# Kernel optimization log

Measured on AMD Instinct MI355X. Metric: run time of the kernel, lower is better.

The kernel has to match this reference:

```python
import jax, jax.numpy as jnp
import numpy as np

B, S, D = 4, 2048, 1024
H, HK = 16, 4          # num_heads, num_heads_kv
HD = D // H            # head_dim = 64
G = H // HK            # kv groups = 4


def setup_inputs() -> dict:
    key = jax.random.key(0)
    ks = jax.random.split(key, 7)
    s = 0.02
    return {
        "query": jax.random.normal(ks[0], (B, S, D), jnp.float32),
        "key":   jax.random.normal(ks[1], (B, S, D), jnp.float32),
        "value": jax.random.normal(ks[2], (B, S, D), jnp.float32),
        # weights stored (in, out); equivalent to torch Linear y = x @ W.T
        "Wq": jax.random.normal(ks[3], (D, H * HD), jnp.float32) * s,
        "Wk": jax.random.normal(ks[4], (D, HK * HD), jnp.float32) * s,
        "Wv": jax.random.normal(ks[5], (D, HK * HD), jnp.float32) * s,
        "Wo": jax.random.normal(ks[6], (H * HD, D), jnp.float32) * s,
    }


def reference(query, key, value, Wq, Wk, Wv, Wo):
    b, qlen, _ = query.shape
    kvlen = key.shape[1]
    # projections
    q = (query @ Wq).reshape(b, qlen, H, HD)        # [b,q,H,hd]
    k = (key @ Wk).reshape(b, kvlen, HK, HD)        # [b,s,HK,hd]
    v = (value @ Wv).reshape(b, kvlen, HK, HD)      # [b,s,HK,hd]
    # GQA: q head h attends kv head h//G (repeat_interleave semantics)
    qg = q.reshape(b, qlen, HK, G, HD)              # head = kv*G + group
    scale = 1.0 / jnp.sqrt(jnp.asarray(HD, q.dtype))
    # scores [b,HK,G,q,s] -- broadcast kv heads, no materialized repeat
    scores = jnp.einsum('bqkgd,bskd->bkgqs', qg, k) * scale
    attn = jax.nn.softmax(scores, axis=-1)
    out = jnp.einsum('bkgqs,bskd->bqkgd', attn, v)  # [b,q,HK,G,hd]
    out = out.reshape(b, qlen, H * HD)
    return out @ Wo
```

## Files before the change

kernel.cpp:

```cpp
#include <hip/hip_runtime.h>


typedef unsigned short u16;
typedef unsigned int   u32;
typedef __bf16 bf16x4 __attribute__((ext_vector_type(4)));
typedef __bf16 bf16x8 __attribute__((ext_vector_type(8)));
typedef float  f32x4  __attribute__((ext_vector_type(4)));

#define MFMA(a,b,c) __builtin_amdgcn_mfma_f32_16x16x32_bf16((a),(b),(c),0,0,0)

#define GLDS(g, l) __builtin_amdgcn_global_load_lds(                          \
    (const __attribute__((address_space(1))) void*)(g),                       \
    (__attribute__((address_space(3))) void*)(l), 16, 0, 0)

#if __has_builtin(__builtin_amdgcn_exp2f)
#define EXP2(x) __builtin_amdgcn_exp2f(x)
#else
#define EXP2(x) exp2f(x)
#endif

__device__ __forceinline__ u16 f2bf(float f){
    u32 u = __builtin_bit_cast(u32, f);
    u += 0x7fffu + ((u >> 16) & 1u);
    return (u16)(u >> 16);
}
__device__ __forceinline__ u32 pk2(float a, float b){
#if __has_builtin(__builtin_amdgcn_cvt_pk_bf16_f32)
    auto r = __builtin_amdgcn_cvt_pk_bf16_f32(a, b);
    return __builtin_bit_cast(u32, r);
#else
    return (u32)f2bf(a) | ((u32)f2bf(b) << 16);
#endif
}
__device__ __forceinline__ bf16x8 ldfrag(const u16* p){
    return *(const bf16x8*)p;
}
__device__ __forceinline__ bf16x8 ld2x64(const u16* p){
    bf16x4 lo = *(const bf16x4*)p;
    bf16x4 hi = *(const bf16x4*)(p + 4);
    bf16x8 r;
    r[0]=lo[0]; r[1]=lo[1]; r[2]=lo[2]; r[3]=lo[3];
    r[4]=hi[0]; r[5]=hi[1]; r[6]=hi[2]; r[7]=hi[3];
    return r;
}

__global__ __launch_bounds__(256) void prep(const float* __restrict__ Wq,
                                            const float* __restrict__ Wk,
                                            const float* __restrict__ Wv,
                                            const float* __restrict__ Wo,
                                            u16* WqT, u16* WkT, u16* WvT, u16* WoT){
    const int tid = threadIdx.x, bid = blockIdx.x;
    __shared__ float T[32][33];
    const float* W; u16* WT; int N, i;
    if (bid < 1024)      { W = Wq; WT = WqT; N = 1024; i = bid; }
    else if (bid < 1280) { W = Wk; WT = WkT; N =  256; i = bid - 1024; }
    else if (bid < 1536) { W = Wv; WT = WvT; N =  256; i = bid - 1280; }
    else                 { W = Wo; WT = WoT; N = 1024; i = bid - 1536; }
    int kt = (i & 31) * 32, nt = (i >> 5) * 32;
    int r = tid >> 3, c = tid & 7;
    float4 vv = *(const float4*)(W + (size_t)(kt + r) * N + nt + c * 4);
    T[r][c*4+0] = vv.x; T[r][c*4+1] = vv.y; T[r][c*4+2] = vv.z; T[r][c*4+3] = vv.w;
    __syncthreads();
    u32 lo = pk2(T[c*4+0][r], T[c*4+1][r]);
    u32 hi = pk2(T[c*4+2][r], T[c*4+3][r]);
    *(uint2*)(WT + (size_t)(nt + r) * 1024 + kt + c * 4) = make_uint2(lo, hi);
}

template<int ATYPE, int EPI>
__device__ __forceinline__ void gemm_body(const void* __restrict__ Ap,
                                          const u16* __restrict__ Bt,
                                          void* __restrict__ Cp,
                                          int N, int K, int m0, int n0,
                                          u16* As, u16* Bs, float oscale){
    constexpr int ASTR = (ATYPE == 0) ? 80 : 64;
    const int tid  = threadIdx.x;
    const int wave = tid >> 6, lane = tid & 63;
    const int quad = lane >> 4, l15 = lane & 15;
    const int wm = wave >> 1, wn = wave & 1;
    const int srow = lane >> 3;
    const int scol = ((lane & 7) ^ srow) * 8;
    const int swz  = l15 & 7;

    f32x4 acc[4][4];
    #pragma unroll
    for (int i = 0; i < 4; ++i)
        #pragma unroll
        for (int j = 0; j < 4; ++j) acc[i][j] = (f32x4){0.f, 0.f, 0.f, 0.f};

    const int nkt = K >> 6;
    for (int kt = 0; kt < nkt; ++kt){
        __syncthreads();
        if constexpr (ATYPE == 0){
            const float* A = (const float*)Ap;
            int c4 = tid & 15, r0 = tid >> 4;
            #pragma unroll
            for (int p = 0; p < 8; ++p){
                int r = r0 + p * 16;
                float4 v = *(const float4*)(A + (size_t)(m0 + r) * K + kt * 64 + c4 * 4);
                *(uint2*)&As[r * 80 + c4 * 4] = make_uint2(pk2(v.x, v.y), pk2(v.z, v.w));
            }
        } else {
            const u16* A = (const u16*)Ap;
            const u16* ga = A + (size_t)(m0 + wave*32 + srow) * K + kt*64 + scol;
            u16* la = As + (wave*32) * 64;
            #pragma unroll
            for (int p = 0; p < 4; ++p)
                GLDS(ga + (size_t)(p*8) * K, la + p*8*64);
        }
        {
            const u16* gb = Bt + (size_t)(n0 + wave*32 + srow) * K + kt*64 + scol;
            u16* lb = Bs + (wave*32) * 64;
            #pragma unroll
            for (int p = 0; p < 4; ++p)
                GLDS(gb + (size_t)(p*8) * K, lb + p*8*64);
        }
        __syncthreads();
        #pragma unroll
        for (int ks = 0; ks < 2; ++ks){
            bf16x8 af[4], bfr[4];
            #pragma unroll
            for (int mt = 0; mt < 4; ++mt){
                if constexpr (ATYPE == 0)
                    af[mt] = ldfrag(&As[(wm*64 + mt*16 + l15) * 80 + ks*32 + quad*8]);
                else
                    af[mt] = ldfrag(&As[(wm*64 + mt*16 + l15) * 64 +
                                        (((ks*4 + quad) ^ swz) * 8)]);
            }
            #pragma unroll
            for (int nt = 0; nt < 4; ++nt)
                bfr[nt] = ldfrag(&Bs[(wn*64 + nt*16 + l15) * 64 +
                                     (((ks*4 + quad) ^ swz) * 8)]);
            #pragma unroll
            for (int mt = 0; mt < 4; ++mt)
                #pragma unroll
                for (int nt = 0; nt < 4; ++nt){
                    if constexpr (EPI == 1)
                        acc[mt][nt] = MFMA(af[mt], bfr[nt], acc[mt][nt]);
                    else
                        acc[mt][nt] = MFMA(bfr[nt], af[mt], acc[mt][nt]);
                }
        }
    }
    #pragma unroll
    for (int mt = 0; mt < 4; ++mt){
        #pragma unroll
        for (int nt = 0; nt < 4; ++nt){
            if constexpr (EPI == 1){
                int rowb = m0 + wm*64 + mt*16 + quad*4;
                int col  = n0 + wn*64 + nt*16 + l15;
                u16* C = (u16*)Cp;
                int bb = rowb >> 11, s = rowb & 2047;
                u32 lo = pk2(acc[mt][nt][0], acc[mt][nt][1]);
                u32 hi = pk2(acc[mt][nt][2], acc[mt][nt][3]);
                *(uint2*)(C + (size_t)(bb * 256 + col) * 2048 + s) = make_uint2(lo, hi);
            } else {
                int row  = m0 + wm*64 + mt*16 + l15;
                int colb = n0 + wn*64 + nt*16 + quad*4;
                if constexpr (EPI == 0){
                    u16* C = (u16*)Cp;
                    u32 lo = pk2(acc[mt][nt][0]*oscale, acc[mt][nt][1]*oscale);
                    u32 hi = pk2(acc[mt][nt][2]*oscale, acc[mt][nt][3]*oscale);
                    *(uint2*)(C + (size_t)row * N + colb) = make_uint2(lo, hi);
                } else {
                    float* C = (float*)Cp;
                    *(f32x4*)(C + (size_t)row * N + colb) = acc[mt][nt];
                }
            }
        }
    }
}

__global__ __launch_bounds__(256) void gemm_qkv(const float* q, const u16* WqT, u16* Qp,
                                                const float* k, const u16* WkT, u16* Kp,
                                                const float* v, const u16* WvT, u16* Vt,
                                                float qscale){
    __shared__ u16 As[128 * 80];
    __shared__ u16 Bs[128 * 64];
    int bid = blockIdx.x;
    if (bid < 512)
        gemm_body<0,0>((const void*)q, WqT, (void*)Qp, 1024, 1024,
                       (bid >> 3) * 128, (bid & 7) * 128, As, Bs, qscale);
    else if (bid < 640){
        int i = bid - 512;
        gemm_body<0,0>((const void*)k, WkT, (void*)Kp, 256, 1024,
                       (i >> 1) * 128, (i & 1) * 128, As, Bs, 1.0f);
    } else {
        int i = bid - 640;
        gemm_body<0,1>((const void*)v, WvT, (void*)Vt, 256, 1024,
                       (i >> 1) * 128, (i & 1) * 128, As, Bs, 1.0f);
    }
}

__global__ __launch_bounds__(256) void gemm_o(const u16* AO, const u16* WoT,
                                              float* Out){
    __shared__ u16 As[128 * 64];
    __shared__ u16 Bs[128 * 64];
    int bid = blockIdx.x;
    gemm_body<1,2>((const void*)AO, WoT, (void*)Out, 1024, 1024,
                   (bid >> 3) * 128, (bid & 7) * 128, As, Bs, 1.0f);
}

__global__ __launch_bounds__(512, 4) void attn_k(const u16* __restrict__ Qp,
                                                 const u16* __restrict__ Kp,
                                                 const u16* __restrict__ Vt,
                                                 u16* __restrict__ AO){
    constexpr int S = 2048, Dm = 1024, NKV = 256, PST = 68;
    __shared__ u16 Kb[2][64 * 64];
    __shared__ u16 Vb[2][64 * 64];
    __shared__ u16 Ps[256 * PST];
    const int tid = threadIdx.x, wave = tid >> 6, lane = tid & 63;
    const int quad = lane >> 4, l15 = lane & 15;
    const int h = blockIdx.y, b = blockIdx.z;
    const int hk = h >> 2, q0 = blockIdx.x * 256;
    u16* pw = Ps + wave * (32 * PST);

    const int srow = lane >> 3;
    const int scol = ((lane & 7) ^ srow) * 8;
    const int swz  = l15 & 7;

    auto issue = [&](int t){
        int j0 = t * 64, bufi = t & 1;
        int r = wave * 8 + srow;
        GLDS(Kp + (size_t)(b * S + j0 + r) * NKV + hk * 64 + scol,
             &Kb[bufi][wave * 8 * 64]);
        GLDS(Vt + (size_t)(b * NKV + hk * 64 + r) * S + j0 + scol,
             &Vb[bufi][wave * 8 * 64]);
    };

    issue(0);
    {
        int c8 = tid & 7, r0 = tid >> 3;
        #pragma unroll
        for (int p = 0; p < 4; ++p){
            int r = r0 + p * 64;
            uint4 v = *(const uint4*)(Qp + (size_t)(b * S + q0 + r) * Dm + h * 64 + c8 * 8);
            *(uint2*)&Ps[r * PST + c8 * 8]     = make_uint2(v.x, v.y);
            *(uint2*)&Ps[r * PST + c8 * 8 + 4] = make_uint2(v.z, v.w);
        }
    }
    __syncthreads();
    bf16x8 qf[2][2];
    #pragma unroll
    for (int mt = 0; mt < 2; ++mt)
        #pragma unroll
        for (int ks = 0; ks < 2; ++ks)
            qf[mt][ks] = ld2x64(&Ps[(wave*32 + mt*16 + l15) * PST + ks*32 + quad*8]);

    const u32 one2 = 0x3F803F80u;
    const bf16x8 ones = __builtin_bit_cast(bf16x8, make_uint4(one2, one2, one2, one2));

    f32x4 O[4][2];
    #pragma unroll
    for (int dt = 0; dt < 4; ++dt)
        #pragma unroll
        for (int mt = 0; mt < 2; ++mt) O[dt][mt] = (f32x4){0.f, 0.f, 0.f, 0.f};
    f32x4 sums[2];
    #pragma unroll
    for (int mt = 0; mt < 2; ++mt) sums[mt] = (f32x4){0.f, 0.f, 0.f, 0.f};

    for (int t = 0; t < 32; ++t){
        __syncthreads();
        if (t < 31) issue(t + 1);
        const u16* Kt = Kb[t & 1];
        const u16* Vs = Vb[t & 1];
        f32x4 sf[2][4];
        #pragma unroll
        for (int mt = 0; mt < 2; ++mt)
            #pragma unroll
            for (int nt = 0; nt < 4; ++nt) sf[mt][nt] = (f32x4){0.f, 0.f, 0.f, 0.f};
        #pragma unroll
        for (int ks = 0; ks < 2; ++ks){
            bf16x8 ak[4];
            #pragma unroll
            for (int nt = 0; nt < 4; ++nt)
                ak[nt] = ldfrag(&Kt[(nt*16 + l15) * 64 + (((ks*4 + quad) ^ swz) * 8)]);
            #pragma unroll
            for (int mt = 0; mt < 2; ++mt)
                #pragma unroll
                for (int nt = 0; nt < 4; ++nt)
                    sf[mt][nt] = MFMA(ak[nt], qf[mt][ks], sf[mt][nt]);
        }
        #pragma unroll
        for (int mt = 0; mt < 2; ++mt)
            #pragma unroll
            for (int nt = 0; nt < 4; ++nt){
                float e0 = EXP2(sf[mt][nt][0]);
                float e1 = EXP2(sf[mt][nt][1]);
                float e2 = EXP2(sf[mt][nt][2]);
                float e3 = EXP2(sf[mt][nt][3]);
                *(uint2*)&pw[(mt*16 + l15) * PST + nt*16 + quad*4] =
                    make_uint2(pk2(e0, e1), pk2(e2, e3));
            }
        __threadfence_block();
        #pragma unroll
        for (int ks = 0; ks < 2; ++ks){
            bf16x8 av[4], bp[2];
            #pragma unroll
            for (int dt = 0; dt < 4; ++dt)
                av[dt] = ldfrag(&Vs[(dt*16 + l15) * 64 + (((ks*4 + quad) ^ swz) * 8)]);
            #pragma unroll
            for (int mt = 0; mt < 2; ++mt)
                bp[mt] = ld2x64(&pw[(mt*16 + l15) * PST + ks*32 + quad*8]);
            #pragma unroll
            for (int mt = 0; mt < 2; ++mt)
                sums[mt] = MFMA(ones, bp[mt], sums[mt]);
            #pragma unroll
            for (int dt = 0; dt < 4; ++dt)
                #pragma unroll
                for (int mt = 0; mt < 2; ++mt)
                    O[dt][mt] = MFMA(av[dt], bp[mt], O[dt][mt]);
        }
    }
    #pragma unroll
    for (int mt = 0; mt < 2; ++mt){
        float inv = 1.0f / sums[mt][0];
        size_t row = (size_t)(b * S + q0 + wave*32 + mt*16 + l15);
        #pragma unroll
        for (int dt = 0; dt < 4; ++dt){
            u32 lo = pk2(O[dt][mt][0] * inv, O[dt][mt][1] * inv);
            u32 hi = pk2(O[dt][mt][2] * inv, O[dt][mt][3] * inv);
            *(uint2*)(AO + row * Dm + h * 64 + dt*16 + quad*4) = make_uint2(lo, hi);
        }
    }
}

extern "C" void kernel_launch(void* const* d_in, const int* in_sizes, int n_in,
                              void* d_out, int out_size, void* d_ws, size_t ws_size,
                              hipStream_t stream){
    const float* q  = (const float*)d_in[0];
    const float* k  = (const float*)d_in[1];
    const float* v  = (const float*)d_in[2];
    const float* Wq = (const float*)d_in[3];
    const float* Wk = (const float*)d_in[4];
    const float* Wv = (const float*)d_in[5];
    const float* Wo = (const float*)d_in[6];
    char* ws = (char*)d_ws;
    const size_t MB = 1u << 20;
    u16* WqT = (u16*)(ws);
    u16* WkT = (u16*)(ws + 2*MB);
    u16* WvT = (u16*)(ws + 2*MB + 512*1024);
    u16* WoT = (u16*)(ws + 3*MB);
    u16* Qp  = (u16*)(ws + 5*MB);
    u16* Kp  = (u16*)(ws + 21*MB);
    u16* Vt  = (u16*)(ws + 25*MB);
    u16* AO  = (u16*)(ws + 29*MB);

    const float cexp = 0.125f * 1.44269504f;

    prep<<<dim3(2560), 256, 0, stream>>>(Wq, Wk, Wv, Wo, WqT, WkT, WvT, WoT);
    gemm_qkv<<<dim3(768), 256, 0, stream>>>(q, WqT, Qp, k, WkT, Kp,
                                            v, WvT, Vt, cexp);
    attn_k<<<dim3(8, 16, 4), 512, 0, stream>>>(Qp, Kp, Vt, AO);
    gemm_o<<<dim3(512), 256, 0, stream>>>(AO, WoT, (float*)d_out);
}
```

Before: 314.2 us.

## Double-buffer GEMM LDS tiles and prefetch next K-tile during MFMA

Converts the projection GEMMs to a double-buffered LDS pipeline: the next K-tile's A (fp32 into registers) and B (global_load_lds) loads are issued before computing on the current tile. The fp32 A tile is converted and written to LDS after the MFMAs, which drops one barrier per iteration. The fp32 A tile also changes from a padded stride-80 layout to the XOR-swizzled stride-64 layout. This hides global load latency behind compute, at the cost of doubled LDS use and 8 extra float4 registers, which may reduce occupancy.

```diff
diff --git a/kernel.cpp b/kernel.cpp
--- a/kernel.cpp
+++ b/kernel.cpp
@@ -72,7 +72,6 @@
                                           void* __restrict__ Cp,
                                           int N, int K, int m0, int n0,
                                           u16* As, u16* Bs, float oscale){
-    constexpr int ASTR = (ATYPE == 0) ? 80 : 64;
     const int tid  = threadIdx.x;
     const int wave = tid >> 6, lane = tid & 63;
     const int quad = lane >> 4, l15 = lane & 15;
@@ -80,6 +79,7 @@
     const int srow = lane >> 3;
     const int scol = ((lane & 7) ^ srow) * 8;
     const int swz  = l15 & 7;
+    const int c4 = tid & 15, r0 = tid >> 4;
 
     f32x4 acc[4][4];
     #pragma unroll
@@ -88,48 +88,64 @@
         for (int j = 0; j < 4; ++j) acc[i][j] = (f32x4){0.f, 0.f, 0.f, 0.f};
 
     const int nkt = K >> 6;
-    for (int kt = 0; kt < nkt; ++kt){
-        __syncthreads();
+    float4 areg[8];
+
+    auto issueA = [&](int kt){
         if constexpr (ATYPE == 0){
             const float* A = (const float*)Ap;
-            int c4 = tid & 15, r0 = tid >> 4;
-            #pragma unroll
-            for (int p = 0; p < 8; ++p){
-                int r = r0 + p * 16;
-                float4 v = *(const float4*)(A + (size_t)(m0 + r) * K + kt * 64 + c4 * 4);
-                *(uint2*)&As[r * 80 + c4 * 4] = make_uint2(pk2(v.x, v.y), pk2(v.z, v.w));
-            }
+            #pragma unroll
+            for (int p = 0; p < 8; ++p)
+                areg[p] = *(const float4*)(A + (size_t)(m0 + r0 + p*16) * K
+                                             + kt*64 + c4*4);
         } else {
             const u16* A = (const u16*)Ap;
             const u16* ga = A + (size_t)(m0 + wave*32 + srow) * K + kt*64 + scol;
-            u16* la = As + (wave*32) * 64;
+            u16* la = As + (kt & 1) * (128*64) + (wave*32) * 64;
             #pragma unroll
             for (int p = 0; p < 4; ++p)
                 GLDS(ga + (size_t)(p*8) * K, la + p*8*64);
         }
-        {
-            const u16* gb = Bt + (size_t)(n0 + wave*32 + srow) * K + kt*64 + scol;
-            u16* lb = Bs + (wave*32) * 64;
-            #pragma unroll
-            for (int p = 0; p < 4; ++p)
-                GLDS(gb + (size_t)(p*8) * K, lb + p*8*64);
-        }
-        __syncthreads();
+    };
+    auto writeA = [&](int kt){
+        u16* dst = As + (kt & 1) * (128*64);
+        #pragma unroll
+        for (int p = 0; p < 8; ++p){
+            int r = r0 + p*16;
+            *(uint2*)&dst[r*64 + (((c4>>1) ^ (r&7))*8 + (c4&1)*4)] =
+                make_uint2(pk2(areg[p].x, areg[p].y), pk2(areg[p].z, areg[p].w));
+        }
+    };
+    auto issueB = [&](int kt){
+        const u16* gb = Bt + (size_t)(n0 + wave*32 + srow) * K + kt*64 + scol;
+        u16* lb = Bs + (kt & 1) * (128*64) + (wave*32) * 64;
+        #pragma unroll
+        for (int p = 0; p < 4; ++p)
+            GLDS(gb + (size_t)(p*8) * K, lb + p*8*64);
+    };
+
+    issueA(0);
+    issueB(0);
+    if constexpr (ATYPE == 0) writeA(0);
+    __syncthreads();
+
+    for (int kt = 0; kt < nkt; ++kt){
+        const u16* Asc = As + (kt & 1) * (128*64);
+        const u16* Bsc = Bs + (kt & 1) * (128*64);
+        if (kt + 1 < nkt){
+            issueA(kt + 1);
+            issueB(kt + 1);
+        }
         #pragma unroll
         for (int ks = 0; ks < 2; ++ks){
             bf16x8 af[4], bfr[4];
             #pragma unroll
-            for (int mt = 0; mt < 4; ++mt){
-                if constexpr (ATYPE == 0)
-                    af[mt] = ldfrag(&As[(wm*64 + mt*16 + l15) * 80 + ks*32 + quad*8]);
-                else
-                    af[mt] = ldfrag(&As[(wm*64 + mt*16 + l15) * 64 +
-                                        (((ks*4 + quad) ^ swz) * 8)]);
-            }
+            for (int mt = 0; mt < 4; ++mt)
+                af[mt] = ldfrag(&Asc[(wm*64 + mt*16 + l15) * 64 +
+                                     (((ks*4 + quad) ^ swz) * 8)]);
             #pragma unroll
             for (int nt = 0; nt < 4; ++nt)
-                bfr[nt] = ldfrag(&Bs[(wn*64 + nt*16 + l15) * 64 +
-                                     (((ks*4 + quad) ^ swz) * 8)]);
+                bfr[nt] = ldfrag(&Bsc[(wn*64 + nt*16 + l15) * 64 +
+                                      (((ks*4 + quad) ^ swz) * 8)]);
             #pragma unroll
             for (int mt = 0; mt < 4; ++mt)
                 #pragma unroll
@@ -140,6 +156,10 @@
                         acc[mt][nt] = MFMA(bfr[nt], af[mt], acc[mt][nt]);
                 }
         }
+        if constexpr (ATYPE == 0){
+            if (kt + 1 < nkt) writeA(kt + 1);
+        }
+        __syncthreads();
     }
     #pragma unroll
     for (int mt = 0; mt < 4; ++mt){
@@ -174,8 +194,8 @@
                                                 const float* k, const u16* WkT, u16* Kp,
                                                 const float* v, const u16* WvT, u16* Vt,
                                                 float qscale){
-    __shared__ u16 As[128 * 80];
-    __shared__ u16 Bs[128 * 64];
+    __shared__ u16 As[2 * 128 * 64];
+    __shared__ u16 Bs[2 * 128 * 64];
     int bid = blockIdx.x;
     if (bid < 512)
         gemm_body<0,0>((const void*)q, WqT, (void*)Qp, 1024, 1024,
@@ -193,8 +213,8 @@
 
 __global__ __launch_bounds__(256) void gemm_o(const u16* AO, const u16* WoT,
                                               float* Out){
-    __shared__ u16 As[128 * 64];
-    __shared__ u16 Bs[128 * 64];
+    __shared__ u16 As[2 * 128 * 64];
+    __shared__ u16 Bs[2 * 128 * 64];
     int bid = blockIdx.x;
     gemm_body<1,2>((const void*)AO, WoT, (void*)Out, 1024, 1024,
                    (bid >> 3) * 128, (bid & 7) * 128, As, Bs, 1.0f);
```

Measured after the change: 332.2 us. 1.06x slower.

## Prefetch fp32 A tiles into registers, swizzle A LDS, remap GEMM blocks

Applied to the files above, without the earlier changes.

The fp32 A operand of the QKV projection GEMM is now loaded into registers one k-tile ahead and written to LDS at the start of the next iteration. This is meant to hide global load latency behind the MFMA work. The A tile in LDS switches from a padded 80-element stride to the same XOR-swizzled 64-element layout as B, which also cuts LDS use. Block indices are remapped so that blocks likely resident on the same XCD share M rows for better L2 reuse, and launch bounds now request 4 blocks per CU. The prefetch adds register pressure, since eight float4 values stay live across the MFMA loop.

```diff
diff --git a/kernel.cpp b/kernel.cpp
--- a/kernel.cpp
+++ b/kernel.cpp
@@ -72,7 +72,6 @@
                                           void* __restrict__ Cp,
                                           int N, int K, int m0, int n0,
                                           u16* As, u16* Bs, float oscale){
-    constexpr int ASTR = (ATYPE == 0) ? 80 : 64;
     const int tid  = threadIdx.x;
     const int wave = tid >> 6, lane = tid & 63;
     const int quad = lane >> 4, l15 = lane & 15;
@@ -80,6 +79,7 @@
     const int srow = lane >> 3;
     const int scol = ((lane & 7) ^ srow) * 8;
     const int swz  = l15 & 7;
+    const int c4 = tid & 15, r0 = tid >> 4;
 
     f32x4 acc[4][4];
     #pragma unroll
@@ -88,17 +88,31 @@
         for (int j = 0; j < 4; ++j) acc[i][j] = (f32x4){0.f, 0.f, 0.f, 0.f};
 
     const int nkt = K >> 6;
+    float4 areg[8];
+
+    auto loadA = [&](int kt){
+        const float* A = (const float*)Ap;
+        #pragma unroll
+        for (int p = 0; p < 8; ++p)
+            areg[p] = *(const float4*)(A + (size_t)(m0 + r0 + p*16) * K
+                                         + kt*64 + c4*4);
+    };
+    auto writeA = [&](){
+        #pragma unroll
+        for (int p = 0; p < 8; ++p){
+            int r = r0 + p*16;
+            *(uint2*)&As[r*64 + (((c4>>1) ^ (r&7))*8 + (c4&1)*4)] =
+                make_uint2(pk2(areg[p].x, areg[p].y), pk2(areg[p].z, areg[p].w));
+        }
+    };
+
+    if constexpr (ATYPE == 0) loadA(0);
+
     for (int kt = 0; kt < nkt; ++kt){
-        __syncthreads();
+        if (kt) __syncthreads();
         if constexpr (ATYPE == 0){
-            const float* A = (const float*)Ap;
-            int c4 = tid & 15, r0 = tid >> 4;
-            #pragma unroll
-            for (int p = 0; p < 8; ++p){
-                int r = r0 + p * 16;
-                float4 v = *(const float4*)(A + (size_t)(m0 + r) * K + kt * 64 + c4 * 4);
-                *(uint2*)&As[r * 80 + c4 * 4] = make_uint2(pk2(v.x, v.y), pk2(v.z, v.w));
-            }
+            writeA();
+            if (kt + 1 < nkt) loadA(kt + 1);
         } else {
             const u16* A = (const u16*)Ap;
             const u16* ga = A + (size_t)(m0 + wave*32 + srow) * K + kt*64 + scol;
@@ -119,13 +133,9 @@
         for (int ks = 0; ks < 2; ++ks){
             bf16x8 af[4], bfr[4];
             #pragma unroll
-            for (int mt = 0; mt < 4; ++mt){
-                if constexpr (ATYPE == 0)
-                    af[mt] = ldfrag(&As[(wm*64 + mt*16 + l15) * 80 + ks*32 + quad*8]);
-                else
-                    af[mt] = ldfrag(&As[(wm*64 + mt*16 + l15) * 64 +
-                                        (((ks*4 + quad) ^ swz) * 8)]);
-            }
+            for (int mt = 0; mt < 4; ++mt)
+                af[mt] = ldfrag(&As[(wm*64 + mt*16 + l15) * 64 +
+                                    (((ks*4 + quad) ^ swz) * 8)]);
             #pragma unroll
             for (int nt = 0; nt < 4; ++nt)
                 bfr[nt] = ldfrag(&Bs[(wn*64 + nt*16 + l15) * 64 +
@@ -170,34 +180,42 @@
     }
 }
 
-__global__ __launch_bounds__(256) void gemm_qkv(const float* q, const u16* WqT, u16* Qp,
-                                                const float* k, const u16* WkT, u16* Kp,
-                                                const float* v, const u16* WvT, u16* Vt,
-                                                float qscale){
-    __shared__ u16 As[128 * 80];
-    __shared__ u16 Bs[128 * 64];
-    int bid = blockIdx.x;
-    if (bid < 512)
-        gemm_body<0,0>((const void*)q, WqT, (void*)Qp, 1024, 1024,
-                       (bid >> 3) * 128, (bid & 7) * 128, As, Bs, qscale);
-    else if (bid < 640){
-        int i = bid - 512;
-        gemm_body<0,0>((const void*)k, WkT, (void*)Kp, 256, 1024,
-                       (i >> 1) * 128, (i & 1) * 128, As, Bs, 1.0f);
-    } else {
-        int i = bid - 640;
-        gemm_body<0,1>((const void*)v, WvT, (void*)Vt, 256, 1024,
-                       (i >> 1) * 128, (i & 1) * 128, As, Bs, 1.0f);
-    }
-}
-
-__global__ __launch_bounds__(256) void gemm_o(const u16* AO, const u16* WoT,
-                                              float* Out){
+__global__ __launch_bounds__(256, 4) void gemm_qkv(const float* q, const u16* WqT, u16* Qp,
+                                                   const float* k, const u16* WkT, u16* Kp,
+                                                   const float* v, const u16* WvT, u16* Vt,
+                                                   float qscale){
     __shared__ u16 As[128 * 64];
     __shared__ u16 Bs[128 * 64];
     int bid = blockIdx.x;
+    if (bid < 512){
+        int x = bid & 7, s = bid >> 3;
+        int m = x * 8 + (s >> 3), n = s & 7;
+        gemm_body<0,0>((const void*)q, WqT, (void*)Qp, 1024, 1024,
+                       m * 128, n * 128, As, Bs, qscale);
+    } else if (bid < 640){
+        int i = bid - 512;
+        int x = i & 7, s = i >> 3;
+        int m = x * 8 + (s >> 1), n = s & 1;
+        gemm_body<0,0>((const void*)k, WkT, (void*)Kp, 256, 1024,
+                       m * 128, n * 128, As, Bs, 1.0f);
+    } else {
+        int i = bid - 640;
+        int x = i & 7, s = i >> 3;
+        int m = x * 8 + (s >> 1), n = s & 1;
+        gemm_body<0,1>((const void*)v, WvT, (void*)Vt, 256, 1024,
+                       m * 128, n * 128, As, Bs, 1.0f);
+    }
+}
+
+__global__ __launch_bounds__(256, 4) void gemm_o(const u16* AO, const u16* WoT,
+                                                 float* Out){
+    __shared__ u16 As[128 * 64];
+    __shared__ u16 Bs[128 * 64];
+    int bid = blockIdx.x;
+    int x = bid & 7, s = bid >> 3;
+    int m = x * 8 + (s >> 3), n = s & 7;
     gemm_body<1,2>((const void*)AO, WoT, (void*)Out, 1024, 1024,
-                   (bid >> 3) * 128, (bid & 7) * 128, As, Bs, 1.0f);
+                   m * 128, n * 128, As, Bs, 1.0f);
 }
 
 __global__ __launch_bounds__(512, 4) void attn_k(const u16* __restrict__ Qp,
```

Result: slower. 326.0 us (+3.8%).

## Shrink GEMM tiles to 128x64, swizzle A smem, remap blocks for XCD locality

Applied to the files above, without the earlier changes.

The projection GEMMs move from 128x128 to 128x64 output tiles, which doubles the grid sizes of gemm_qkv and gemm_o so more blocks can run at once on the many CUs. The fp32 A tile is now stored with an XOR swizzle instead of a padded stride, so both A paths share one fragment-load form. Block indices are remapped so that consecutive blocks going to the same XCD share A rows, aiming for better L2 reuse. The first barrier is also skipped. In exchange, each block gets less operand reuse per tile and the total global reads of A go up.

```diff
diff --git a/kernel.cpp b/kernel.cpp
--- a/kernel.cpp
+++ b/kernel.cpp
@@ -72,7 +72,6 @@
                                           void* __restrict__ Cp,
                                           int N, int K, int m0, int n0,
                                           u16* As, u16* Bs, float oscale){
-    constexpr int ASTR = (ATYPE == 0) ? 80 : 64;
     const int tid  = threadIdx.x;
     const int wave = tid >> 6, lane = tid & 63;
     const int quad = lane >> 4, l15 = lane & 15;
@@ -80,60 +79,55 @@
     const int srow = lane >> 3;
     const int scol = ((lane & 7) ^ srow) * 8;
     const int swz  = l15 & 7;
-
-    f32x4 acc[4][4];
+    const int c4 = tid & 15, r0 = tid >> 4;
+
+    f32x4 acc[4][2];
     #pragma unroll
     for (int i = 0; i < 4; ++i)
         #pragma unroll
-        for (int j = 0; j < 4; ++j) acc[i][j] = (f32x4){0.f, 0.f, 0.f, 0.f};
+        for (int j = 0; j < 2; ++j) acc[i][j] = (f32x4){0.f, 0.f, 0.f, 0.f};
 
     const int nkt = K >> 6;
     for (int kt = 0; kt < nkt; ++kt){
-        __syncthreads();
+        if (kt) __syncthreads();
         if constexpr (ATYPE == 0){
             const float* A = (const float*)Ap;
-            int c4 = tid & 15, r0 = tid >> 4;
             #pragma unroll
             for (int p = 0; p < 8; ++p){
                 int r = r0 + p * 16;
-                float4 v = *(const float4*)(A + (size_t)(m0 + r) * K + kt * 64 + c4 * 4);
-                *(uint2*)&As[r * 80 + c4 * 4] = make_uint2(pk2(v.x, v.y), pk2(v.z, v.w));
+                float4 v = *(const float4*)(A + (size_t)(m0 + r) * K + kt*64 + c4*4);
+                *(uint2*)&As[r*64 + (((c4>>1) ^ (r&7))*8 + (c4&1)*4)] =
+                    make_uint2(pk2(v.x, v.y), pk2(v.z, v.w));
             }
         } else {
             const u16* A = (const u16*)Ap;
             const u16* ga = A + (size_t)(m0 + wave*32 + srow) * K + kt*64 + scol;
-            u16* la = As + (wave*32) * 64;
             #pragma unroll
             for (int p = 0; p < 4; ++p)
-                GLDS(ga + (size_t)(p*8) * K, la + p*8*64);
+                GLDS(ga + (size_t)(p*8) * K, As + (wave*32 + p*8) * 64);
         }
         {
-            const u16* gb = Bt + (size_t)(n0 + wave*32 + srow) * K + kt*64 + scol;
-            u16* lb = Bs + (wave*32) * 64;
-            #pragma unroll
-            for (int p = 0; p < 4; ++p)
-                GLDS(gb + (size_t)(p*8) * K, lb + p*8*64);
+            const u16* gb = Bt + (size_t)(n0 + wave*16 + srow) * K + kt*64 + scol;
+            #pragma unroll
+            for (int p = 0; p < 2; ++p)
+                GLDS(gb + (size_t)(p*8) * K, Bs + (wave*16 + p*8) * 64);
         }
         __syncthreads();
         #pragma unroll
         for (int ks = 0; ks < 2; ++ks){
-            bf16x8 af[4], bfr[4];
-            #pragma unroll
-            for (int mt = 0; mt < 4; ++mt){
-                if constexpr (ATYPE == 0)
-                    af[mt] = ldfrag(&As[(wm*64 + mt*16 + l15) * 80 + ks*32 + quad*8]);
-                else
-                    af[mt] = ldfrag(&As[(wm*64 + mt*16 + l15) * 64 +
-                                        (((ks*4 + quad) ^ swz) * 8)]);
-            }
-            #pragma unroll
-            for (int nt = 0; nt < 4; ++nt)
-                bfr[nt] = ldfrag(&Bs[(wn*64 + nt*16 + l15) * 64 +
+            bf16x8 af[4], bfr[2];
+            #pragma unroll
+            for (int mt = 0; mt < 4; ++mt)
+                af[mt] = ldfrag(&As[(wm*64 + mt*16 + l15) * 64 +
+                                    (((ks*4 + quad) ^ swz) * 8)]);
+            #pragma unroll
+            for (int nt = 0; nt < 2; ++nt)
+                bfr[nt] = ldfrag(&Bs[(wn*32 + nt*16 + l15) * 64 +
                                      (((ks*4 + quad) ^ swz) * 8)]);
             #pragma unroll
             for (int mt = 0; mt < 4; ++mt)
                 #pragma unroll
-                for (int nt = 0; nt < 4; ++nt){
+                for (int nt = 0; nt < 2; ++nt){
                     if constexpr (EPI == 1)
                         acc[mt][nt] = MFMA(af[mt], bfr[nt], acc[mt][nt]);
                     else
@@ -144,10 +138,10 @@
     #pragma unroll
     for (int mt = 0; mt < 4; ++mt){
         #pragma unroll
-        for (int nt = 0; nt < 4; ++nt){
+        for (int nt = 0; nt < 2; ++nt){
             if constexpr (EPI == 1){
                 int rowb = m0 + wm*64 + mt*16 + quad*4;
-                int col  = n0 + wn*64 + nt*16 + l15;
+                int col  = n0 + wn*32 + nt*16 + l15;
                 u16* C = (u16*)Cp;
                 int bb = rowb >> 11, s = rowb & 2047;
                 u32 lo = pk2(acc[mt][nt][0], acc[mt][nt][1]);
@@ -155,7 +149,7 @@
                 *(uint2*)(C + (size_t)(bb * 256 + col) * 2048 + s) = make_uint2(lo, hi);
             } else {
                 int row  = m0 + wm*64 + mt*16 + l15;
-                int colb = n0 + wn*64 + nt*16 + quad*4;
+                int colb = n0 + wn*32 + nt*16 + quad*4;
                 if constexpr (EPI == 0){
                     u16* C = (u16*)Cp;
                     u32 lo = pk2(acc[mt][nt][0]*oscale, acc[mt][nt][1]*oscale);
@@ -174,30 +168,38 @@
                                                 const float* k, const u16* WkT, u16* Kp,
                                                 const float* v, const u16* WvT, u16* Vt,
                                                 float qscale){
-    __shared__ u16 As[128 * 80];
-    __shared__ u16 Bs[128 * 64];
+    __shared__ u16 As[128 * 64];
+    __shared__ u16 Bs[64 * 64];
     int bid = blockIdx.x;
-    if (bid < 512)
+    if (bid < 1024){
+        int x = bid & 7, s = bid >> 3;
+        int m = x * 8 + (s >> 4), n = s & 15;
         gemm_body<0,0>((const void*)q, WqT, (void*)Qp, 1024, 1024,
-                       (bid >> 3) * 128, (bid & 7) * 128, As, Bs, qscale);
-    else if (bid < 640){
-        int i = bid - 512;
+                       m * 128, n * 64, As, Bs, qscale);
+    } else if (bid < 1280){
+        int i = bid - 1024;
+        int x = i & 7, s = i >> 3;
+        int m = x * 8 + (s >> 2), n = s & 3;
         gemm_body<0,0>((const void*)k, WkT, (void*)Kp, 256, 1024,
-                       (i >> 1) * 128, (i & 1) * 128, As, Bs, 1.0f);
+                       m * 128, n * 64, As, Bs, 1.0f);
     } else {
-        int i = bid - 640;
+        int i = bid - 1280;
+        int x = i & 7, s = i >> 3;
+        int m = x * 8 + (s >> 2), n = s & 3;
         gemm_body<0,1>((const void*)v, WvT, (void*)Vt, 256, 1024,
-                       (i >> 1) * 128, (i & 1) * 128, As, Bs, 1.0f);
+                       m * 128, n * 64, As, Bs, 1.0f);
     }
 }
 
 __global__ __launch_bounds__(256) void gemm_o(const u16* AO, const u16* WoT,
                                               float* Out){
     __shared__ u16 As[128 * 64];
-    __shared__ u16 Bs[128 * 64];
+    __shared__ u16 Bs[64 * 64];
     int bid = blockIdx.x;
+    int x = bid & 7, s = bid >> 3;
+    int m = x * 8 + (s >> 4), n = s & 15;
     gemm_body<1,2>((const void*)AO, WoT, (void*)Out, 1024, 1024,
-                   (bid >> 3) * 128, (bid & 7) * 128, As, Bs, 1.0f);
+                   m * 128, n * 64, As, Bs, 1.0f);
 }
 
 __global__ __launch_bounds__(512, 4) void attn_k(const u16* __restrict__ Qp,
@@ -348,8 +350,8 @@
     const float cexp = 0.125f * 1.44269504f;
 
     prep<<<dim3(2560), 256, 0, stream>>>(Wq, Wk, Wv, Wo, WqT, WkT, WvT, WoT);
-    gemm_qkv<<<dim3(768), 256, 0, stream>>>(q, WqT, Qp, k, WkT, Kp,
-                                            v, WvT, Vt, cexp);
+    gemm_qkv<<<dim3(1536), 256, 0, stream>>>(q, WqT, Qp, k, WkT, Kp,
+                                             v, WvT, Vt, cexp);
     attn_k<<<dim3(8, 16, 4), 512, 0, stream>>>(Qp, Kp, Vt, AO);
-    gemm_o<<<dim3(512), 256, 0, stream>>>(AO, WoT, (float*)d_out);
-}
+    gemm_o<<<dim3(1024), 256, 0, stream>>>(AO, WoT, (float*)d_out);
+}
```

Result: slower. 405.6 us (+29.1%).
